# Kernel optimization log

Hardware: AMD Instinct MI355X
Metric: run time of the kernel (lower is better)

## Reference

```python
import jax, jax.numpy as jnp
import numpy as np

GRID_SIZE = 5
SPLINE_ORDER = 3
GRID_LO, GRID_HI = -1.0, 1.0
N_BASIS = GRID_SIZE + SPLINE_ORDER  # 8


def make_grid():
    # Extended knot vector as in efficient-kan: grid_size+2*spline_order+1 points
    h = (GRID_HI - GRID_LO) / GRID_SIZE
    return (jnp.arange(-SPLINE_ORDER, GRID_SIZE + SPLINE_ORDER + 1, dtype=jnp.float32) * h + GRID_LO)  # (12,)


def b_splines(x, grid):
    # Cox-de Boor recursion; x: (...,) -> (..., N_BASIS)
    xg = x[..., None]
    bases = ((xg >= grid[:-1]) & (xg < grid[1:])).astype(x.dtype)
    for k in range(1, SPLINE_ORDER + 1):
        left = (xg - grid[: -(k + 1)]) / (grid[k:-1] - grid[: -(k + 1)]) * bases[..., :-1]
        right = (grid[k + 1:] - xg) / (grid[k + 1:] - grid[1:-k]) * bases[..., 1:]
        bases = left + right
    return bases


def extract_patches3(x):
    # x: (B, C, H, W) -> (B, C, 9, H, W); 3x3 kernel, stride 1, padding 1
    B, C, H, W = x.shape
    xp = jnp.pad(x, ((0, 0), (0, 0), (1, 1), (1, 1)))
    return jnp.stack([xp[:, :, di:di + H, dj:dj + W]
                      for di in range(3) for dj in range(3)], axis=2)


def kan_conv(x, base_w, spline_w, scaler, grid):
    # One KANLinear(9 -> 1) per (out_ch, in_ch) pair, summed over in_ch.
    p = extract_patches3(x)                          # (B, Cin, 9, H, W)
    base = jnp.einsum('biphw,oip->bohw', jax.nn.silu(p), base_w)
    basis = b_splines(p, grid)                       # (B, Cin, 9, H, W, G)
    sw = spline_w * scaler[..., None]                # standalone spline scaler
    spl = jnp.einsum('biphwg,oipg->bohw', basis, sw)
    return base + spl


def maxpool2(x):
    B, C, H, W = x.shape
    return x.reshape(B, C, H // 2, 2, W // 2, 2).max(axis=(3, 5))


def setup_inputs() -> dict:
    key = jax.random.key(0)
    ks = jax.random.split(key, 7)
    return {
        'x': jax.random.normal(ks[0], (2048, 1, 28, 28), dtype=jnp.float32),
        'base_w1': jax.random.normal(ks[1], (2, 1, 9), dtype=jnp.float32) * 0.3,
        'spline_w1': jax.random.normal(ks[2], (2, 1, 9, 8), dtype=jnp.float32) * 0.1,
        'scaler1': jax.random.normal(ks[3], (2, 1, 9), dtype=jnp.float32) * 0.3 + 1.0,
        'base_w2': jax.random.normal(ks[4], (2, 2, 9), dtype=jnp.float32) * 0.3,
        'spline_w2': jax.random.normal(ks[5], (2, 2, 9, 8), dtype=jnp.float32) * 0.1,
        'scaler2': jax.random.normal(ks[6], (2, 2, 9), dtype=jnp.float32) * 0.3 + 1.0,
    }


def reference(x, base_w1, spline_w1, scaler1, base_w2, spline_w2, scaler2):
    grid = make_grid()
    h = maxpool2(kan_conv(x, base_w1, spline_w1, scaler1, grid))   # (B, 2, 14, 14)
    h = maxpool2(kan_conv(h, base_w2, spline_w2, scaler2, grid))   # (B, 2, 7, 7)
    return h.reshape(h.shape[0], -1)                               # (B, 98)
```

## Files before the change

### kernel.cpp

```cpp
#include <hip/hip_runtime.h>
#include <math.h>

typedef _Float16 half_t;
typedef _Float16 h2 __attribute__((ext_vector_type(2)));
typedef unsigned int uint;
typedef unsigned long long u64;

#define TPB 256

__device__ __forceinline__ uint pack_h2f(float a, float b) {
  half_t ha = (half_t)a, hb = (half_t)b;
  unsigned short ua = __builtin_bit_cast(unsigned short, ha);
  unsigned short ub = __builtin_bit_cast(unsigned short, hb);
  return (uint)ua | ((uint)ub << 16);
}

__device__ __forceinline__ float dot8(uint d0, uint d1, uint d2, uint d3,
                                      float sv, const uint* __restrict__ w,
                                      float acc) {
  acc = fmaf(sv, __uint_as_float(w[4]), acc);
#if __has_builtin(__builtin_amdgcn_fdot2)
  acc = __builtin_amdgcn_fdot2(__builtin_bit_cast(h2, d0), __builtin_bit_cast(h2, w[0]), acc, false);
  acc = __builtin_amdgcn_fdot2(__builtin_bit_cast(h2, d1), __builtin_bit_cast(h2, w[1]), acc, false);
  acc = __builtin_amdgcn_fdot2(__builtin_bit_cast(h2, d2), __builtin_bit_cast(h2, w[2]), acc, false);
  acc = __builtin_amdgcn_fdot2(__builtin_bit_cast(h2, d3), __builtin_bit_cast(h2, w[3]), acc, false);
#else
  uint dd[4] = {d0, d1, d2, d3};
#pragma unroll
  for (int k = 0; k < 4; ++k) {
    h2 f = __builtin_bit_cast(h2, dd[k]);
    h2 wv = __builtin_bit_cast(h2, w[k]);
    acc = fmaf((float)f.x, (float)wv.x, acc);
    acc = fmaf((float)f.y, (float)wv.y, acc);
  }
#endif
  return acc;
}

__device__ __forceinline__ void feat_store(float x, uint* __restrict__ A,
                                           uint* __restrict__ Bq,
                                           uint* __restrict__ S) {
  float e = __expf(-x);
  float silu = x * __builtin_amdgcn_rcpf(1.0f + e);
  float s = fmaf(x, 2.5f, 5.5f);
  float sf = floorf(s);
  float t = s - sf;
  int p = (int)sf - 3;
  float omt = 1.0f - t, t2 = t * t;
  float B0 = (1.0f / 6.0f) * omt * omt * omt;
  float B3 = (1.0f / 6.0f) * t2 * t;
  float B1 = fmaf(0.5f * t, t2, 2.0f / 3.0f - t2);
  float B2 = 1.0f - B0 - B1 - B3;
  u64 Av = ((u64)pack_h2f(B2, B3) << 32) | pack_h2f(B0, B1);
  int n = p < 0 ? -p : 0;
  Av = (n >= 4) ? 0ull : (Av >> (16 * n));
  int pc = p < 0 ? 0 : (p > 9 ? 9 : p);
  int sh = 16 * pc;
  u64 lo = (sh < 64) ? (Av << sh) : 0ull;
  u64 hi = (sh == 0) ? 0ull
         : (sh < 64) ? (Av >> (64 - sh))
         : (sh < 128) ? (Av << (sh - 64)) : 0ull;
  *(uint2*)A = make_uint2((uint)lo, (uint)(lo >> 32));
  *(uint2*)Bq = make_uint2((uint)hi, (uint)(hi >> 32));
  *S = __float_as_uint(silu);
}

__global__ void pack_w(const float* __restrict__ bw1, const float* __restrict__ sw1,
                       const float* __restrict__ sc1, const float* __restrict__ bw2,
                       const float* __restrict__ sw2, const float* __restrict__ sc2,
                       uint* __restrict__ W) {
  const int t = threadIdx.x;
  if (t < 18) {
    const float scv = sc1[t];
    uint* dst = W + t * 5;
#pragma unroll
    for (int j = 0; j < 4; ++j)
      dst[j] = pack_h2f(sw1[t * 8 + 2 * j] * scv, sw1[t * 8 + 2 * j + 1] * scv);
    dst[4] = __float_as_uint(bw1[t]);
  } else if (t < 54) {
    const int q = t - 18;
    const float scv = sc2[q];
    uint* dst = W + 90 + q * 5;
#pragma unroll
    for (int j = 0; j < 4; ++j)
      dst[j] = pack_h2f(sw2[q * 8 + 2 * j] * scv, sw2[q * 8 + 2 * j + 1] * scv);
    dst[4] = __float_as_uint(bw2[q]);
  }
}

__global__ __launch_bounds__(TPB, 5) void kan_fwd(
    const float* __restrict__ x, const uint* __restrict__ W,
    float* __restrict__ out)
{
  __shared__ __align__(16) uint lds[6460];
  uint* F1A = lds;
  uint* F1B = lds + 1800;
  uint* F1S = lds + 3600;
  uint* F2A = lds + 4500;
  uint* F2B = lds + 5284;
  uint* F2S = lds + 6068;
  float* P = (float*)lds;

  const int tid = threadIdx.x;
  const float* xb = x + (size_t)blockIdx.x * 784;

  for (int ii = tid; ii < 900; ii += TPB) {
    int hp = ii >= 450 ? 1 : 0;
    int k = ii - hp * 450;
    int r = k / 15, cc = k % 15;
    int c = 2 * cc + hp;
    bool inter = ((uint)(r - 1) < 28u) && ((uint)(c - 1) < 28u);
    int xi = (r - 1) * 28 + (c - 1);
    xi = min(max(xi, 0), 783);
    float xv = xb[xi];
    xv = inter ? xv : 0.0f;
    int sidx = r * 30 + cc + hp * 15;
    feat_store(xv, F1A + sidx * 2, F1B + sidx * 2, F1S + sidx);
  }
  __syncthreads();

  if (tid < 196) {
    const int ph = tid / 14, pw = tid % 14;
    float acc[2][4];
#pragma unroll
    for (int o = 0; o < 2; ++o)
#pragma unroll
      for (int q = 0; q < 4; ++q) acc[o][q] = 0.0f;
#pragma unroll
    for (int r = 0; r < 4; ++r) {
#pragma unroll
      for (int c = 0; c < 4; ++c) {
        const int sidx = (2 * ph + r) * 30 + (pw + (c >> 1)) + (c & 1) * 15;
        uint2 a = *(const uint2*)(F1A + sidx * 2);
        uint2 bq = *(const uint2*)(F1B + sidx * 2);
        float sv = __uint_as_float(F1S[sidx]);
#pragma unroll
        for (int dh = 0; dh < 2; ++dh) {
          if (r - dh < 0 || r - dh > 2) continue;
#pragma unroll
          for (int dw = 0; dw < 2; ++dw) {
            if (c - dw < 0 || c - dw > 2) continue;
            const int tap = (r - dh) * 3 + (c - dw);
#pragma unroll
            for (int o = 0; o < 2; ++o)
              acc[o][dh * 2 + dw] =
                  dot8(a.x, a.y, bq.x, bq.y, sv, W + (o * 9 + tap) * 5, acc[o][dh * 2 + dw]);
          }
        }
      }
    }
#pragma unroll
    for (int o = 0; o < 2; ++o) {
      float m = fmaxf(fmaxf(acc[o][0], acc[o][1]), fmaxf(acc[o][2], acc[o][3]));
      int fidx = o * 196 + ph * 14 + (pw >> 1) + (pw & 1) * 7;
      feat_store(m, F2A + fidx * 2, F2B + fidx * 2, F2S + fidx);
    }
  }
  __syncthreads();

  {
    const int wid = __builtin_amdgcn_readfirstlane(tid >> 6);
    const int lane = tid & 63;
    const uint F0d1 = pack_h2f(1.0f / 48.0f, 23.0f / 48.0f);
    const uint F0d2 = pack_h2f(23.0f / 48.0f, 1.0f / 48.0f);
    if (lane < 49) {
      const int ci = wid & 1;
      const int ph = lane / 7, pw = lane % 7;
      float pa[4] = {0.0f, 0.0f, 0.0f, 0.0f};
#pragma unroll
      for (int r = 0; r < 4; ++r) {
#pragma unroll
        for (int c = 0; c < 4; ++c) {
          int row = 2 * ph + r - 1, col = 2 * pw + c - 1;
          bool ok = ((uint)row < 14u) && ((uint)col < 14u);
          int rcl = min(max(row, 0), 13), ccl = min(max(col, 0), 13);
          const int fidx = ci * 196 + rcl * 14 + (ccl >> 1) + (ccl & 1) * 7;
          uint2 a = *(const uint2*)(F2A + fidx * 2);
          uint2 bq = *(const uint2*)(F2B + fidx * 2);
          float sv = ok ? __uint_as_float(F2S[fidx]) : 0.0f;
          uint d0 = ok ? a.x : 0u;
          uint d1 = ok ? a.y : F0d1;
          uint d2 = ok ? bq.x : F0d2;
          uint d3 = ok ? bq.y : 0u;
#pragma unroll
          for (int dh = 0; dh < 2; ++dh) {
            if (r - dh < 0 || r - dh > 2) continue;
#pragma unroll
            for (int dw = 0; dw < 2; ++dw) {
              if (c - dw < 0 || c - dw > 2) continue;
              const int tap = (r - dh) * 3 + (c - dw);
              pa[dh * 2 + dw] =
                  dot8(d0, d1, d2, d3, sv, W + 90 + (wid * 9 + tap) * 5, pa[dh * 2 + dw]);
            }
          }
        }
      }
      *(float4*)&P[(wid * 49 + lane) * 4] = make_float4(pa[0], pa[1], pa[2], pa[3]);
    }
  }
  __syncthreads();

  if (tid < 98) {
    const int o = tid / 49, pos = tid % 49;
    const float4 p0 = *(const float4*)&P[((o * 2 + 0) * 49 + pos) * 4];
    const float4 p1 = *(const float4*)&P[((o * 2 + 1) * 49 + pos) * 4];
    float m = fmaxf(fmaxf(p0.x + p1.x, p0.y + p1.y), fmaxf(p0.z + p1.z, p0.w + p1.w));
    out[(size_t)blockIdx.x * 98 + tid] = m;
  }
}

extern "C" void kernel_launch(void* const* d_in, const int* in_sizes, int n_in,
                              void* d_out, int out_size, void* d_ws, size_t ws_size,
                              hipStream_t stream) {
  const float* x   = (const float*)d_in[0];
  const float* bw1 = (const float*)d_in[1];
  const float* sw1 = (const float*)d_in[2];
  const float* sc1 = (const float*)d_in[3];
  const float* bw2 = (const float*)d_in[4];
  const float* sw2 = (const float*)d_in[5];
  const float* sc2 = (const float*)d_in[6];
  float* out = (float*)d_out;
  uint* W = (uint*)d_ws;
  const int B = in_sizes[0] / 784;
  pack_w<<<1, 64, 0, stream>>>(bw1, sw1, sc1, bw2, sw2, sc2, W);
  kan_fwd<<<B, TPB, 0, stream>>>(x, W, out);
}
```

Before: 86.46 us.

## Fuse weight packing into main kernel and stage weights in LDS/registers

Removes the separate pack_w launch: each block now packs the scaled spline and base weights itself into a small LDS region. Each thread then loads its layer's 48-word weight slice from LDS into registers with vector loads, instead of issuing scalar global loads per dot product. Layer 1 is restructured to loop over output channels, keeping one channel's weights live at a time to limit register pressure. This trades one kernel launch and many global weight loads for redundant per-block packing, larger LDS use and more registers.

Measured after the change: 120.7 us. +39.6%, slower.

```diff
diff --git a/kernel.cpp b/kernel.cpp
--- a/kernel.cpp
+++ b/kernel.cpp
@@ -15,9 +15,9 @@
   return (uint)ua | ((uint)ub << 16);
 }
 
-__device__ __forceinline__ float dot8(uint d0, uint d1, uint d2, uint d3,
-                                      float sv, const uint* __restrict__ w,
-                                      float acc) {
+__device__ __forceinline__ float dot8r(uint d0, uint d1, uint d2, uint d3,
+                                       float sv, const uint* __restrict__ w,
+                                       float acc) {
   acc = fmaf(sv, __uint_as_float(w[4]), acc);
 #if __has_builtin(__builtin_amdgcn_fdot2)
   acc = __builtin_amdgcn_fdot2(__builtin_bit_cast(h2, d0), __builtin_bit_cast(h2, w[0]), acc, false);
@@ -65,44 +65,44 @@
   *S = __float_as_uint(silu);
 }
 
-__global__ void pack_w(const float* __restrict__ bw1, const float* __restrict__ sw1,
-                       const float* __restrict__ sc1, const float* __restrict__ bw2,
-                       const float* __restrict__ sw2, const float* __restrict__ sc2,
-                       uint* __restrict__ W) {
-  const int t = threadIdx.x;
-  if (t < 18) {
-    const float scv = sc1[t];
-    uint* dst = W + t * 5;
-#pragma unroll
-    for (int j = 0; j < 4; ++j)
-      dst[j] = pack_h2f(sw1[t * 8 + 2 * j] * scv, sw1[t * 8 + 2 * j + 1] * scv);
-    dst[4] = __float_as_uint(bw1[t]);
-  } else if (t < 54) {
-    const int q = t - 18;
-    const float scv = sc2[q];
-    uint* dst = W + 90 + q * 5;
-#pragma unroll
-    for (int j = 0; j < 4; ++j)
-      dst[j] = pack_h2f(sw2[q * 8 + 2 * j] * scv, sw2[q * 8 + 2 * j + 1] * scv);
-    dst[4] = __float_as_uint(bw2[q]);
-  }
-}
-
 __global__ __launch_bounds__(TPB, 5) void kan_fwd(
-    const float* __restrict__ x, const uint* __restrict__ W,
+    const float* __restrict__ x,
+    const float* __restrict__ bw1, const float* __restrict__ sw1,
+    const float* __restrict__ sc1, const float* __restrict__ bw2,
+    const float* __restrict__ sw2, const float* __restrict__ sc2,
     float* __restrict__ out)
 {
-  __shared__ __align__(16) uint lds[6460];
+  __shared__ __align__(16) uint lds[6748];
   uint* F1A = lds;
   uint* F1B = lds + 1800;
   uint* F1S = lds + 3600;
   uint* F2A = lds + 4500;
   uint* F2B = lds + 5284;
   uint* F2S = lds + 6068;
+  uint* Wl  = lds + 6460;
   float* P = (float*)lds;
 
   const int tid = threadIdx.x;
   const float* xb = x + (size_t)blockIdx.x * 784;
+
+  if (tid < 54) {
+    if (tid < 18) {
+      const float scv = sc1[tid];
+      uint* dst = Wl + (tid / 9) * 48 + (tid % 9) * 5;
+#pragma unroll
+      for (int j = 0; j < 4; ++j)
+        dst[j] = pack_h2f(sw1[tid * 8 + 2 * j] * scv, sw1[tid * 8 + 2 * j + 1] * scv);
+      dst[4] = __float_as_uint(bw1[tid]);
+    } else {
+      const int q = tid - 18;
+      const float scv = sc2[q];
+      uint* dst = Wl + 96 + (q / 9) * 48 + (q % 9) * 5;
+#pragma unroll
+      for (int j = 0; j < 4; ++j)
+        dst[j] = pack_h2f(sw2[q * 8 + 2 * j] * scv, sw2[q * 8 + 2 * j + 1] * scv);
+      dst[4] = __float_as_uint(bw2[q]);
+    }
+  }
 
   for (int ii = tid; ii < 900; ii += TPB) {
     int hp = ii >= 450 ? 1 : 0;
@@ -121,37 +121,35 @@
 
   if (tid < 196) {
     const int ph = tid / 14, pw = tid % 14;
-    float acc[2][4];
-#pragma unroll
-    for (int o = 0; o < 2; ++o)
-#pragma unroll
-      for (int q = 0; q < 4; ++q) acc[o][q] = 0.0f;
-#pragma unroll
-    for (int r = 0; r < 4; ++r) {
-#pragma unroll
-      for (int c = 0; c < 4; ++c) {
-        const int sidx = (2 * ph + r) * 30 + (pw + (c >> 1)) + (c & 1) * 15;
-        uint2 a = *(const uint2*)(F1A + sidx * 2);
-        uint2 bq = *(const uint2*)(F1B + sidx * 2);
-        float sv = __uint_as_float(F1S[sidx]);
-#pragma unroll
-        for (int dh = 0; dh < 2; ++dh) {
-          if (r - dh < 0 || r - dh > 2) continue;
-#pragma unroll
-          for (int dw = 0; dw < 2; ++dw) {
-            if (c - dw < 0 || c - dw > 2) continue;
-            const int tap = (r - dh) * 3 + (c - dw);
-#pragma unroll
-            for (int o = 0; o < 2; ++o)
-              acc[o][dh * 2 + dw] =
-                  dot8(a.x, a.y, bq.x, bq.y, sv, W + (o * 9 + tap) * 5, acc[o][dh * 2 + dw]);
+#pragma unroll
+    for (int o = 0; o < 2; ++o) {
+      uint wv[48];
+#pragma unroll
+      for (int k = 0; k < 12; ++k)
+        *(uint4*)&wv[k * 4] = *(const uint4*)(Wl + o * 48 + k * 4);
+      float acc[4] = {0.0f, 0.0f, 0.0f, 0.0f};
+#pragma unroll
+      for (int r = 0; r < 4; ++r) {
+#pragma unroll
+        for (int c = 0; c < 4; ++c) {
+          const int sidx = (2 * ph + r) * 30 + (pw + (c >> 1)) + (c & 1) * 15;
+          uint2 a = *(const uint2*)(F1A + sidx * 2);
+          uint2 bq = *(const uint2*)(F1B + sidx * 2);
+          float sv = __uint_as_float(F1S[sidx]);
+#pragma unroll
+          for (int dh = 0; dh < 2; ++dh) {
+            if (r - dh < 0 || r - dh > 2) continue;
+#pragma unroll
+            for (int dw = 0; dw < 2; ++dw) {
+              if (c - dw < 0 || c - dw > 2) continue;
+              const int tap = (r - dh) * 3 + (c - dw);
+              acc[dh * 2 + dw] =
+                  dot8r(a.x, a.y, bq.x, bq.y, sv, &wv[tap * 5], acc[dh * 2 + dw]);
+            }
           }
         }
       }
-    }
-#pragma unroll
-    for (int o = 0; o < 2; ++o) {
-      float m = fmaxf(fmaxf(acc[o][0], acc[o][1]), fmaxf(acc[o][2], acc[o][3]));
+      float m = fmaxf(fmaxf(acc[0], acc[1]), fmaxf(acc[2], acc[3]));
       int fidx = o * 196 + ph * 14 + (pw >> 1) + (pw & 1) * 7;
       feat_store(m, F2A + fidx * 2, F2B + fidx * 2, F2S + fidx);
     }
@@ -166,6 +164,10 @@
     if (lane < 49) {
       const int ci = wid & 1;
       const int ph = lane / 7, pw = lane % 7;
+      uint wv[48];
+#pragma unroll
+      for (int k = 0; k < 12; ++k)
+        *(uint4*)&wv[k * 4] = *(const uint4*)(Wl + 96 + wid * 48 + k * 4);
       float pa[4] = {0.0f, 0.0f, 0.0f, 0.0f};
 #pragma unroll
       for (int r = 0; r < 4; ++r) {
@@ -190,7 +192,7 @@
               if (c - dw < 0 || c - dw > 2) continue;
               const int tap = (r - dh) * 3 + (c - dw);
               pa[dh * 2 + dw] =
-                  dot8(d0, d1, d2, d3, sv, W + 90 + (wid * 9 + tap) * 5, pa[dh * 2 + dw]);
+                  dot8r(d0, d1, d2, d3, sv, &wv[tap * 5], pa[dh * 2 + dw]);
             }
           }
         }
@@ -220,8 +222,6 @@
   const float* sw2 = (const float*)d_in[5];
   const float* sc2 = (const float*)d_in[6];
   float* out = (float*)d_out;
-  uint* W = (uint*)d_ws;
   const int B = in_sizes[0] / 784;
-  pack_w<<<1, 64, 0, stream>>>(bw1, sw1, sc1, bw2, sw2, sc2, W);
-  kan_fwd<<<B, TPB, 0, stream>>>(x, W, out);
-}
+  kan_fwd<<<B, TPB, 0, stream>>>(x, bw1, sw1, sc1, bw2, sw2, sc2, out);
+}
```

## Pad weight records to 32B for vector loads, batch stage-1 input loads, raise occupancy

Applied to the files above, without the earlier changes.

Each per-tap weight record grows from 5 to 8 dwords, so the four packed spline weights come in as one aligned uint4 load plus one scalar load instead of five scalar loads. The stage-1 feature loop is unrolled so a thread issues all of its global input loads before doing the spline math, which hides memory latency. The launch-bounds occupancy hint goes from 5 to 6 blocks per CU, which may force tighter register allocation or spills. The larger weight buffer in workspace also costs a bit more scalar-cache footprint.

After: 93.58 us. 8.2% more time.

```diff
diff --git a/kernel.cpp b/kernel.cpp
--- a/kernel.cpp
+++ b/kernel.cpp
@@ -15,21 +15,21 @@
   return (uint)ua | ((uint)ub << 16);
 }
 
-__device__ __forceinline__ float dot8(uint d0, uint d1, uint d2, uint d3,
-                                      float sv, const uint* __restrict__ w,
-                                      float acc) {
-  acc = fmaf(sv, __uint_as_float(w[4]), acc);
+__device__ __forceinline__ float dot8v(uint d0, uint d1, uint d2, uint d3,
+                                       float sv, uint4 wa, uint wb, float acc) {
+  acc = fmaf(sv, __uint_as_float(wb), acc);
 #if __has_builtin(__builtin_amdgcn_fdot2)
-  acc = __builtin_amdgcn_fdot2(__builtin_bit_cast(h2, d0), __builtin_bit_cast(h2, w[0]), acc, false);
-  acc = __builtin_amdgcn_fdot2(__builtin_bit_cast(h2, d1), __builtin_bit_cast(h2, w[1]), acc, false);
-  acc = __builtin_amdgcn_fdot2(__builtin_bit_cast(h2, d2), __builtin_bit_cast(h2, w[2]), acc, false);
-  acc = __builtin_amdgcn_fdot2(__builtin_bit_cast(h2, d3), __builtin_bit_cast(h2, w[3]), acc, false);
+  acc = __builtin_amdgcn_fdot2(__builtin_bit_cast(h2, d0), __builtin_bit_cast(h2, wa.x), acc, false);
+  acc = __builtin_amdgcn_fdot2(__builtin_bit_cast(h2, d1), __builtin_bit_cast(h2, wa.y), acc, false);
+  acc = __builtin_amdgcn_fdot2(__builtin_bit_cast(h2, d2), __builtin_bit_cast(h2, wa.z), acc, false);
+  acc = __builtin_amdgcn_fdot2(__builtin_bit_cast(h2, d3), __builtin_bit_cast(h2, wa.w), acc, false);
 #else
   uint dd[4] = {d0, d1, d2, d3};
+  uint ww[4] = {wa.x, wa.y, wa.z, wa.w};
 #pragma unroll
   for (int k = 0; k < 4; ++k) {
     h2 f = __builtin_bit_cast(h2, dd[k]);
-    h2 wv = __builtin_bit_cast(h2, w[k]);
+    h2 wv = __builtin_bit_cast(h2, ww[k]);
     acc = fmaf((float)f.x, (float)wv.x, acc);
     acc = fmaf((float)f.y, (float)wv.y, acc);
   }
@@ -65,6 +65,20 @@
   *S = __float_as_uint(silu);
 }
 
+__device__ __forceinline__ float s1_load(const float* __restrict__ xb, int ii,
+                                         int& sidx) {
+  int hp = ii >= 450 ? 1 : 0;
+  int k = ii - hp * 450;
+  int r = k / 15, cc = k % 15;
+  int c = 2 * cc + hp;
+  bool inter = ((uint)(r - 1) < 28u) && ((uint)(c - 1) < 28u);
+  int xi = (r - 1) * 28 + (c - 1);
+  xi = min(max(xi, 0), 783);
+  float xv = xb[xi];
+  sidx = r * 30 + cc + hp * 15;
+  return inter ? xv : 0.0f;
+}
+
 __global__ void pack_w(const float* __restrict__ bw1, const float* __restrict__ sw1,
                        const float* __restrict__ sc1, const float* __restrict__ bw2,
                        const float* __restrict__ sw2, const float* __restrict__ sc2,
@@ -72,7 +86,7 @@
   const int t = threadIdx.x;
   if (t < 18) {
     const float scv = sc1[t];
-    uint* dst = W + t * 5;
+    uint* dst = W + t * 8;
 #pragma unroll
     for (int j = 0; j < 4; ++j)
       dst[j] = pack_h2f(sw1[t * 8 + 2 * j] * scv, sw1[t * 8 + 2 * j + 1] * scv);
@@ -80,7 +94,7 @@
   } else if (t < 54) {
     const int q = t - 18;
     const float scv = sc2[q];
-    uint* dst = W + 90 + q * 5;
+    uint* dst = W + t * 8;
 #pragma unroll
     for (int j = 0; j < 4; ++j)
       dst[j] = pack_h2f(sw2[q * 8 + 2 * j] * scv, sw2[q * 8 + 2 * j + 1] * scv);
@@ -88,7 +102,7 @@
   }
 }
 
-__global__ __launch_bounds__(TPB, 5) void kan_fwd(
+__global__ __launch_bounds__(TPB, 6) void kan_fwd(
     const float* __restrict__ x, const uint* __restrict__ W,
     float* __restrict__ out)
 {
@@ -104,18 +118,17 @@
   const int tid = threadIdx.x;
   const float* xb = x + (size_t)blockIdx.x * 784;
 
-  for (int ii = tid; ii < 900; ii += TPB) {
-    int hp = ii >= 450 ? 1 : 0;
-    int k = ii - hp * 450;
-    int r = k / 15, cc = k % 15;
-    int c = 2 * cc + hp;
-    bool inter = ((uint)(r - 1) < 28u) && ((uint)(c - 1) < 28u);
-    int xi = (r - 1) * 28 + (c - 1);
-    xi = min(max(xi, 0), 783);
-    float xv = xb[xi];
-    xv = inter ? xv : 0.0f;
-    int sidx = r * 30 + cc + hp * 15;
-    feat_store(xv, F1A + sidx * 2, F1B + sidx * 2, F1S + sidx);
+  {
+    int s0, s1i, s2i, s3i;
+    const bool has3 = tid < (900 - 768);
+    float x0 = s1_load(xb, tid, s0);
+    float x1 = s1_load(xb, tid + 256, s1i);
+    float x2 = s1_load(xb, tid + 512, s2i);
+    float x3 = s1_load(xb, has3 ? tid + 768 : tid, s3i);
+    feat_store(x0, F1A + s0 * 2, F1B + s0 * 2, F1S + s0);
+    feat_store(x1, F1A + s1i * 2, F1B + s1i * 2, F1S + s1i);
+    feat_store(x2, F1A + s2i * 2, F1B + s2i * 2, F1S + s2i);
+    if (has3) feat_store(x3, F1A + s3i * 2, F1B + s3i * 2, F1S + s3i);
   }
   __syncthreads();
 
@@ -142,9 +155,12 @@
             if (c - dw < 0 || c - dw > 2) continue;
             const int tap = (r - dh) * 3 + (c - dw);
 #pragma unroll
-            for (int o = 0; o < 2; ++o)
+            for (int o = 0; o < 2; ++o) {
+              const uint4 wa = *(const uint4*)(W + (o * 9 + tap) * 8);
+              const uint wb = W[(o * 9 + tap) * 8 + 4];
               acc[o][dh * 2 + dw] =
-                  dot8(a.x, a.y, bq.x, bq.y, sv, W + (o * 9 + tap) * 5, acc[o][dh * 2 + dw]);
+                  dot8v(a.x, a.y, bq.x, bq.y, sv, wa, wb, acc[o][dh * 2 + dw]);
+            }
           }
         }
       }
@@ -189,8 +205,10 @@
             for (int dw = 0; dw < 2; ++dw) {
               if (c - dw < 0 || c - dw > 2) continue;
               const int tap = (r - dh) * 3 + (c - dw);
+              const uint4 wa = *(const uint4*)(W + (18 + wid * 9 + tap) * 8);
+              const uint wb = W[(18 + wid * 9 + tap) * 8 + 4];
               pa[dh * 2 + dw] =
-                  dot8(d0, d1, d2, d3, sv, W + 90 + (wid * 9 + tap) * 5, pa[dh * 2 + dw]);
+                  dot8v(d0, d1, d2, d3, sv, wa, wb, pa[dh * 2 + dw]);
             }
           }
         }
```
